# Kernel optimization log

Measured on AMD Instinct MI355X. Metric: run time of the kernel, lower is better.

## Reference

```python
import jax, jax.numpy as jnp
import numpy as np


def setup_inputs() -> dict:
    key = jax.random.key(0)
    ks = jax.random.split(key, 5)
    B, DEC, ENC, H = 4, 256, 256, 512  # feature_dim = hl_size = 512, mlp hidden = 512
    decoder_states = jax.random.normal(ks[0], (B, DEC, H), dtype=jnp.float32)
    encoder_states = jax.random.normal(ks[1], (B, ENC, H), dtype=jnp.float32)
    ext_mask = jnp.zeros((B, DEC, ENC), dtype=bool)  # self.mask set externally; all-False here
    W_mlp = jax.random.normal(ks[2], (2 * H, H), dtype=jnp.float32) * 0.02  # Linear(2H -> H)
    b_mlp = jnp.zeros((H,), dtype=jnp.float32)
    W_out = jax.random.normal(ks[3], (H, 1), dtype=jnp.float32) * 0.02  # Linear(H -> 1)
    b_out = jnp.zeros((1,), dtype=jnp.float32)
    return {"decoder_states": decoder_states, "encoder_states": encoder_states,
            "ext_mask": ext_mask, "W_mlp": W_mlp, "b_mlp": b_mlp,
            "W_out": W_out, "b_out": b_out}


def reference(decoder_states, encoder_states, ext_mask, W_mlp, b_mlp, W_out, b_out):
    # decoder_states: [B, dec, H]; encoder_states: [B, enc, H]
    H = encoder_states.shape[-1]
    # pad mask: positions where encoder feature-0 equals 0.0 -> [B, 1, enc]
    pad_mask = (encoder_states == 0.0)[:, :, :1]
    pad_mask = jnp.swapaxes(pad_mask, 1, 2)  # [B, 1, enc]
    # cat(enc, dec) @ W_mlp  ==  enc @ W_mlp[:H] + dec @ W_mlp[H:]  (avoids 2H concat)
    enc_proj = jnp.einsum('beh,hm->bem', encoder_states, W_mlp[:H])   # [B, enc, Hm]
    dec_proj = jnp.einsum('bdh,hm->bdm', decoder_states, W_mlp[H:])   # [B, dec, Hm]
    hidden = jnp.tanh(dec_proj[:, :, None, :] + enc_proj[:, None, :, :] + b_mlp)  # [B, dec, enc, Hm]
    attn = jnp.einsum('bdem,mo->bde', hidden, W_out) + b_out[0]       # [B, dec, enc]
    attn = jnp.where(ext_mask, -jnp.inf, attn)
    attn = jnp.where(pad_mask, -jnp.inf, attn)
    attn = jax.nn.softmax(attn, axis=-1)
    context = jnp.einsum('bde,beh->bdh', attn, encoder_states)        # [B, dec, H]
    return (context, attn)
```

## Files before the change

### kernel.cpp

```cpp
#include <hip/hip_runtime.h>
#include <math.h>

#define B 4
#define DEC 256
#define ENC 256
#define HDIM 512

#define TANH_SCALE 2.8853900817779268f
#define LOG2E 1.4426950408889634f

__device__ __forceinline__ float fast_exp2(float x) { return __builtin_amdgcn_exp2f(x); }
__device__ __forceinline__ float fast_rcp(float x)  { return __builtin_amdgcn_rcpf(x); }

typedef __attribute__((ext_vector_type(8))) short bf16x8;
typedef __attribute__((ext_vector_type(4))) short bf16x4;
typedef __attribute__((ext_vector_type(4))) float f32x4;

__device__ __forceinline__ unsigned short bf16_rne(float x) {
    unsigned u = __float_as_uint(x);
    return (unsigned short)((u + 0x7FFFu + ((u >> 16) & 1u)) >> 16);
}
__device__ __forceinline__ float bf16_to_f(unsigned short h) {
    return __uint_as_float((unsigned)h << 16);
}

#define W_OFS(m, k) ((((long)(m) >> 4) << 13) + (((long)(k) >> 3) << 7) + (((m) & 15) << 3) + ((k) & 7))

__global__ __launch_bounds__(256) void convert_kernel(
    const float* __restrict__ enc, const float* __restrict__ dec,
    const float* __restrict__ Wmlp,
    unsigned short* __restrict__ Xh_e, unsigned short* __restrict__ Xl_e,
    unsigned short* __restrict__ Xh_d, unsigned short* __restrict__ Xl_d,
    unsigned short* __restrict__ Wh_e, unsigned short* __restrict__ Wl_e,
    unsigned short* __restrict__ Wh_d, unsigned short* __restrict__ Wl_d)
{
    const int tid = threadIdx.x, z = blockIdx.z;
    if (z < 2) {
        const float* X = z ? dec : enc;
        unsigned short* H = z ? Xh_d : Xh_e;
        unsigned short* L = z ? Xl_d : Xl_e;
        const long i8 = ((long)blockIdx.x * 256 + tid) * 8;
        float4 v0 = *(const float4*)(X + i8);
        float4 v1 = *(const float4*)(X + i8 + 4);
        float xs[8] = {v0.x, v0.y, v0.z, v0.w, v1.x, v1.y, v1.z, v1.w};
        bf16x8 hv, lv;
#pragma unroll
        for (int j = 0; j < 8; ++j) {
            unsigned short h = bf16_rne(xs[j]);
            hv[j] = (short)h;
            lv[j] = (short)bf16_rne(xs[j] - bf16_to_f(h));
        }
        *(bf16x8*)(H + i8) = hv;
        *(bf16x8*)(L + i8) = lv;
    } else {
        const float* Wsrc = Wmlp + (z == 3 ? (long)HDIM * HDIM : 0);
        unsigned short* H = (z == 3) ? Wh_d : Wh_e;
        unsigned short* L = (z == 3) ? Wl_d : Wl_e;
        const int t = blockIdx.x * 256 + tid;
        const int m = t & 511;
        const int k0 = (t >> 9) << 2;
        bf16x4 hv, lv;
#pragma unroll
        for (int j = 0; j < 4; ++j) {
            float x = Wsrc[(long)(k0 + j) * 512 + m];
            unsigned short h = bf16_rne(x);
            hv[j] = (short)h;
            lv[j] = (short)bf16_rne(x - bf16_to_f(h));
        }
        const long ofs = W_OFS(m, k0);
        *(bf16x4*)(H + ofs) = hv;
        *(bf16x4*)(L + ofs) = lv;
    }
}

__global__ __launch_bounds__(256) void proj_mfma_kernel(
    const unsigned short* __restrict__ Xh_e, const unsigned short* __restrict__ Xl_e,
    const unsigned short* __restrict__ Xh_d, const unsigned short* __restrict__ Xl_d,
    const unsigned short* __restrict__ Wh_e, const unsigned short* __restrict__ Wl_e,
    const unsigned short* __restrict__ Wh_d, const unsigned short* __restrict__ Wl_d,
    const float* __restrict__ bmlp,
    float* __restrict__ ET, float* __restrict__ Dmat)
{
    const int tid = threadIdx.x;
    const int wave = tid >> 6, lane = tid & 63;
    const int z = blockIdx.z;
    const int r0w = blockIdx.x * 64 + wave * 16;
    const int m0 = blockIdx.y * 32;
    const unsigned short* Xh = z ? Xh_d : Xh_e;
    const unsigned short* Xl = z ? Xl_d : Xl_e;
    const unsigned short* Wh = z ? Wh_d : Wh_e;
    const unsigned short* Wl = z ? Wl_d : Wl_e;

    const int col = lane & 15;
    const int quad = lane >> 4;

    const unsigned short* pah = Xh + (long)(r0w + col) * 512 + quad * 8;
    const unsigned short* pal = Xl + (long)(r0w + col) * 512 + quad * 8;
    const long bofs = ((long)(m0 >> 4) << 13) + (quad << 7) + (col << 3);
    const unsigned short* pb0h = Wh + bofs;
    const unsigned short* pb0l = Wl + bofs;
    const unsigned short* pb1h = Wh + bofs + 8192;
    const unsigned short* pb1l = Wl + bofs + 8192;

    f32x4 a0h = {0.f,0.f,0.f,0.f}, a0x = {0.f,0.f,0.f,0.f};
    f32x4 a1h = {0.f,0.f,0.f,0.f}, a1x = {0.f,0.f,0.f,0.f};

    bf16x8 Ah = *(const bf16x8*)pah,  Al = *(const bf16x8*)pal;
    bf16x8 B0h = *(const bf16x8*)pb0h, B0l = *(const bf16x8*)pb0l;
    bf16x8 B1h = *(const bf16x8*)pb1h, B1l = *(const bf16x8*)pb1l;

#pragma unroll 1
    for (int k0 = 0; k0 < 512; k0 += 32) {
        bf16x8 nAh = Ah, nAl = Al, nB0h = B0h, nB0l = B0l, nB1h = B1h, nB1l = B1l;
        if (k0 + 32 < 512) {
            nAh = *(const bf16x8*)(pah + k0 + 32);
            nAl = *(const bf16x8*)(pal + k0 + 32);
            const long ko = (long)(k0 + 32) << 4;
            nB0h = *(const bf16x8*)(pb0h + ko);
            nB0l = *(const bf16x8*)(pb0l + ko);
            nB1h = *(const bf16x8*)(pb1h + ko);
            nB1l = *(const bf16x8*)(pb1l + ko);
        }
        a0h = __builtin_amdgcn_mfma_f32_16x16x32_bf16(Ah, B0h, a0h, 0, 0, 0);
        a1h = __builtin_amdgcn_mfma_f32_16x16x32_bf16(Ah, B1h, a1h, 0, 0, 0);
        a0x = __builtin_amdgcn_mfma_f32_16x16x32_bf16(Ah, B0l, a0x, 0, 0, 0);
        a1x = __builtin_amdgcn_mfma_f32_16x16x32_bf16(Ah, B1l, a1x, 0, 0, 0);
        a0x = __builtin_amdgcn_mfma_f32_16x16x32_bf16(Al, B0h, a0x, 0, 0, 0);
        a1x = __builtin_amdgcn_mfma_f32_16x16x32_bf16(Al, B1h, a1x, 0, 0, 0);
        Ah = nAh; Al = nAl; B0h = nB0h; B0l = nB0l; B1h = nB1h; B1l = nB1l;
    }

    if (z == 0) {
        const int batch = r0w >> 8;
        const int e0 = (r0w & 255) + quad * 4;
        float* base = ET + (long)batch * HDIM * ENC;
        float4 v;
        v.x = fast_exp2((a0h[0] + a0x[0]) * TANH_SCALE);
        v.y = fast_exp2((a0h[1] + a0x[1]) * TANH_SCALE);
        v.z = fast_exp2((a0h[2] + a0x[2]) * TANH_SCALE);
        v.w = fast_exp2((a0h[3] + a0x[3]) * TANH_SCALE);
        *(float4*)&base[(long)(m0 + col) * ENC + e0] = v;
        v.x = fast_exp2((a1h[0] + a1x[0]) * TANH_SCALE);
        v.y = fast_exp2((a1h[1] + a1x[1]) * TANH_SCALE);
        v.z = fast_exp2((a1h[2] + a1x[2]) * TANH_SCALE);
        v.w = fast_exp2((a1h[3] + a1x[3]) * TANH_SCALE);
        *(float4*)&base[(long)(m0 + 16 + col) * ENC + e0] = v;
    } else {
        const float bq0 = bmlp[m0 + col];
        const float bq1 = bmlp[m0 + 16 + col];
        const int r = r0w + quad * 4;
#pragma unroll
        for (int i = 0; i < 4; ++i) {
            Dmat[(long)(r + i) * HDIM + m0 + col] =
                fast_exp2((a0h[i] + a0x[i] + bq0) * TANH_SCALE);
            Dmat[(long)(r + i) * HDIM + m0 + 16 + col] =
                fast_exp2((a1h[i] + a1x[i] + bq1) * TANH_SCALE);
        }
    }
}

__global__ __launch_bounds__(512) void attn_ctx_kernel(
    const float* __restrict__ Dmat, const float* __restrict__ ET,
    const float* __restrict__ wo,
    const float* __restrict__ enc, const unsigned char* __restrict__ extm,
    float* __restrict__ attn_out, float* __restrict__ ctx)
{
    __shared__ __align__(16) float ds[4][HDIM];
    __shared__ __align__(16) float wos[HDIM];
    __shared__ __align__(16) float p8[8][4][ENC];
    __shared__ __align__(16) float as4T[ENC][4];
    __shared__ float redm[4][4];
    __shared__ float reds[4][4];

    const int tid = threadIdx.x;
    const int b = blockIdx.z, d0 = blockIdx.x * 4;
    const long g0 = (long)b * DEC + d0;

    ((float4*)ds)[tid] = ((const float4*)(Dmat + g0 * HDIM))[tid];
    if (tid < 128) ((float4*)wos)[tid] = ((const float4*)wo)[tid];

    const int mg = tid >> 6;
    const int e4 = (tid & 63) * 4;
    const int mbase = mg * 64;
    const float* ep = ET + (long)b * HDIM * ENC + (long)mbase * ENC + e4;

    float4 E0 = *(const float4*)(ep);
    float4 E1 = *(const float4*)(ep + ENC);
    __syncthreads();

    float acc[4][4] = {};
    for (int i = 0; i < 64; i += 2) {
        float4 Ea = E0, Eb = E1;
        if (i + 2 < 64) {
            E0 = *(const float4*)(ep + (long)(i + 2) * ENC);
            E1 = *(const float4*)(ep + (long)(i + 3) * ENC);
        }
        const int m = mbase + i;
        const float w0 = wos[m], w1 = wos[m + 1];
#pragma unroll
        for (int r = 0; r < 4; ++r) {
            const float dr0 = ds[r][m];
            const float dr1 = ds[r][m + 1];
#pragma unroll
            for (int j = 0; j < 4; ++j) {
                float ea = ((const float*)&Ea)[j];
                float eb = ((const float*)&Eb)[j];
                acc[r][j] = fmaf(w0, fast_rcp(fmaf(ea, dr0, 1.0f)), acc[r][j]);
                acc[r][j] = fmaf(w1, fast_rcp(fmaf(eb, dr1, 1.0f)), acc[r][j]);
            }
        }
    }
#pragma unroll
    for (int r = 0; r < 4; ++r) {
        float4 v = make_float4(acc[r][0], acc[r][1], acc[r][2], acc[r][3]);
        *(float4*)&p8[mg][r][e4] = v;
    }
    __syncthreads();

    const int ty = tid >> 8;
    const int e = tid & 255;
    const int wave = tid >> 6, lane = tid & 63;

    const bool pad = (enc[((long)b * ENC + e) * HDIM] == 0.0f);
    float l[2], p[2];
#pragma unroll
    for (int rl = 0; rl < 2; ++rl) {
        const int r = ty * 2 + rl;
        float a = 0.f;
#pragma unroll
        for (int q = 0; q < 8; ++q) a += p8[q][r][e];
        const bool xm = extm[(g0 + r) * ENC + e] != 0;
        l[rl] = (pad || xm) ? -__builtin_inff() : -2.0f * a;
    }
    float mx[2] = {l[0], l[1]};
#pragma unroll
    for (int off = 32; off >= 1; off >>= 1) {
#pragma unroll
        for (int rl = 0; rl < 2; ++rl)
            mx[rl] = fmaxf(mx[rl], __shfl_xor(mx[rl], off, 64));
    }
    if (lane == 0) {
        redm[ty * 2 + 0][wave & 3] = mx[0];
        redm[ty * 2 + 1][wave & 3] = mx[1];
    }
    __syncthreads();
    float s[2];
#pragma unroll
    for (int rl = 0; rl < 2; ++rl) {
        const int r = ty * 2 + rl;
        const float gm = fmaxf(fmaxf(redm[r][0], redm[r][1]),
                               fmaxf(redm[r][2], redm[r][3]));
        p[rl] = fast_exp2((l[rl] - gm) * LOG2E);
        s[rl] = p[rl];
    }
#pragma unroll
    for (int off = 32; off >= 1; off >>= 1) {
#pragma unroll
        for (int rl = 0; rl < 2; ++rl)
            s[rl] += __shfl_xor(s[rl], off, 64);
    }
    if (lane == 0) {
        reds[ty * 2 + 0][wave & 3] = s[0];
        reds[ty * 2 + 1][wave & 3] = s[1];
    }
    __syncthreads();
#pragma unroll
    for (int rl = 0; rl < 2; ++rl) {
        const int r = ty * 2 + rl;
        const float gs = reds[r][0] + reds[r][1] + reds[r][2] + reds[r][3];
        const float pr = p[rl] * fast_rcp(gs);
        attn_out[(g0 + r) * ENC + e] = pr;
        as4T[e][r] = pr;
    }
    __syncthreads();

    const int h = tid;
    const float* eh = enc + (long)b * ENC * HDIM + h;
    float ac0 = 0.f, ac1 = 0.f, ac2 = 0.f, ac3 = 0.f;
    float ebuf[8], nbuf[8];
#pragma unroll
    for (int j = 0; j < 8; ++j) ebuf[j] = eh[(long)j * HDIM];
    for (int e0 = 0; e0 < ENC; e0 += 8) {
        if (e0 + 8 < ENC) {
#pragma unroll
            for (int j = 0; j < 8; ++j) nbuf[j] = eh[(long)(e0 + 8 + j) * HDIM];
        }
#pragma unroll
        for (int j = 0; j < 8; ++j) {
            float4 prv = *(const float4*)&as4T[e0 + j][0];
            float ev4 = ebuf[j];
            ac0 = fmaf(prv.x, ev4, ac0);
            ac1 = fmaf(prv.y, ev4, ac1);
            ac2 = fmaf(prv.z, ev4, ac2);
            ac3 = fmaf(prv.w, ev4, ac3);
        }
#pragma unroll
        for (int j = 0; j < 8; ++j) ebuf[j] = nbuf[j];
    }
    ctx[(g0 + 0) * HDIM + h] = ac0;
    ctx[(g0 + 1) * HDIM + h] = ac1;
    ctx[(g0 + 2) * HDIM + h] = ac2;
    ctx[(g0 + 3) * HDIM + h] = ac3;
}

extern "C" void kernel_launch(void* const* d_in, const int* in_sizes, int n_in,
                              void* d_out, int out_size, void* d_ws, size_t ws_size,
                              hipStream_t stream) {
    const float* dec = (const float*)d_in[0];
    const float* enc = (const float*)d_in[1];
    const unsigned char* extm = (const unsigned char*)d_in[2];
    const float* Wmlp = (const float*)d_in[3];
    const float* bmlp = (const float*)d_in[4];
    const float* Wout = (const float*)d_in[5];

    float* ctx = (float*)d_out;
    float* attn = ctx + (size_t)B * DEC * HDIM;

    const size_t F = (size_t)B * DEC * HDIM;
    float* ET = (float*)d_ws;
    float* Dmat = ET + F;
    unsigned short* Xh_e = (unsigned short*)(Dmat + F);
    unsigned short* Xl_e = Xh_e + F;
    unsigned short* Xh_d = Xl_e + F;
    unsigned short* Xl_d = Xh_d + F;
    unsigned short* Wh_e = Xl_d + F;
    unsigned short* Wl_e = Wh_e + HDIM * HDIM;
    unsigned short* Wh_d = Wl_e + HDIM * HDIM;
    unsigned short* Wl_d = Wh_d + HDIM * HDIM;

    convert_kernel<<<dim3(256, 1, 4), 256, 0, stream>>>(
        enc, dec, Wmlp, Xh_e, Xl_e, Xh_d, Xl_d, Wh_e, Wl_e, Wh_d, Wl_d);
    proj_mfma_kernel<<<dim3(16, 16, 2), 256, 0, stream>>>(
        Xh_e, Xl_e, Xh_d, Xl_d, Wh_e, Wl_e, Wh_d, Wl_d, bmlp, ET, Dmat);
    attn_ctx_kernel<<<dim3(DEC / 4, 1, B), 512, 0, stream>>>(
        Dmat, ET, Wout, enc, extm, attn, ctx);
}
```

Before: 116.1 us.

## Split context GEMV over encoder quarters with float4 loads and rotate chunk order

The context stage now gives each thread four hidden columns over one quarter of the encoder positions, loading encoder rows as float4. Partial sums go into the reused shared buffer and are then reduced across the four quarters, replacing per-thread scalar strided loads over all 256 positions. The score loop gets deeper prefetch (four rows in flight) and float2 shared loads. Both loops rotate their chunk start by block index to spread concurrent blocks across memory, at the cost of more registers and an extra barrier.

```diff
diff --git a/kernel.cpp b/kernel.cpp
--- a/kernel.cpp
+++ b/kernel.cpp
@@ -167,7 +167,7 @@
 {
     __shared__ __align__(16) float ds[4][HDIM];
     __shared__ __align__(16) float wos[HDIM];
-    __shared__ __align__(16) float p8[8][4][ENC];
+    __shared__ __align__(16) float pbuf[8][4][ENC];
     __shared__ __align__(16) float as4T[ENC][4];
     __shared__ float redm[4][4];
     __shared__ float reds[4][4];
@@ -175,45 +175,48 @@
     const int tid = threadIdx.x;
     const int b = blockIdx.z, d0 = blockIdx.x * 4;
     const long g0 = (long)b * DEC + d0;
+    const int rot = blockIdx.x >> 3;
 
     ((float4*)ds)[tid] = ((const float4*)(Dmat + g0 * HDIM))[tid];
     if (tid < 128) ((float4*)wos)[tid] = ((const float4*)wo)[tid];
 
-    const int mg = tid >> 6;
+    const int mg = ((tid >> 6) + rot) & 7;
     const int e4 = (tid & 63) * 4;
     const int mbase = mg * 64;
     const float* ep = ET + (long)b * HDIM * ENC + (long)mbase * ENC + e4;
 
-    float4 E0 = *(const float4*)(ep);
-    float4 E1 = *(const float4*)(ep + ENC);
+    float4 Eb0 = *(const float4*)(ep);
+    float4 Eb1 = *(const float4*)(ep + ENC);
+    float4 Eb2 = *(const float4*)(ep + 2 * ENC);
+    float4 Eb3 = *(const float4*)(ep + 3 * ENC);
     __syncthreads();
 
     float acc[4][4] = {};
     for (int i = 0; i < 64; i += 2) {
-        float4 Ea = E0, Eb = E1;
-        if (i + 2 < 64) {
-            E0 = *(const float4*)(ep + (long)(i + 2) * ENC);
-            E1 = *(const float4*)(ep + (long)(i + 3) * ENC);
+        float4 Ea = Eb0, Eb = Eb1;
+        Eb0 = Eb2; Eb1 = Eb3;
+        if (i + 4 < 64) {
+            Eb2 = *(const float4*)(ep + (long)(i + 4) * ENC);
+            Eb3 = *(const float4*)(ep + (long)(i + 5) * ENC);
         }
         const int m = mbase + i;
-        const float w0 = wos[m], w1 = wos[m + 1];
+        const float2 w2 = *(const float2*)&wos[m];
 #pragma unroll
         for (int r = 0; r < 4; ++r) {
-            const float dr0 = ds[r][m];
-            const float dr1 = ds[r][m + 1];
+            const float2 d2 = *(const float2*)&ds[r][m];
 #pragma unroll
             for (int j = 0; j < 4; ++j) {
                 float ea = ((const float*)&Ea)[j];
                 float eb = ((const float*)&Eb)[j];
-                acc[r][j] = fmaf(w0, fast_rcp(fmaf(ea, dr0, 1.0f)), acc[r][j]);
-                acc[r][j] = fmaf(w1, fast_rcp(fmaf(eb, dr1, 1.0f)), acc[r][j]);
+                acc[r][j] = fmaf(w2.x, fast_rcp(fmaf(ea, d2.x, 1.0f)), acc[r][j]);
+                acc[r][j] = fmaf(w2.y, fast_rcp(fmaf(eb, d2.y, 1.0f)), acc[r][j]);
             }
         }
     }
 #pragma unroll
     for (int r = 0; r < 4; ++r) {
         float4 v = make_float4(acc[r][0], acc[r][1], acc[r][2], acc[r][3]);
-        *(float4*)&p8[mg][r][e4] = v;
+        *(float4*)&pbuf[mg][r][e4] = v;
     }
     __syncthreads();
 
@@ -228,7 +231,7 @@
         const int r = ty * 2 + rl;
         float a = 0.f;
 #pragma unroll
-        for (int q = 0; q < 8; ++q) a += p8[q][r][e];
+        for (int q = 0; q < 8; ++q) a += pbuf[q][r][e];
         const bool xm = extm[(g0 + r) * ENC + e] != 0;
         l[rl] = (pad || xm) ? -__builtin_inff() : -2.0f * a;
     }
@@ -274,33 +277,50 @@
     }
     __syncthreads();
 
+    float (*p4c)[4][HDIM] = (float (*)[4][HDIM])pbuf;
+
+    const int hq = (tid & 127) * 4;
+    const int eq = ((tid >> 7) + rot) & 3;
+    const int ebase = eq * 64;
+    const float* ew = enc + (long)b * ENC * HDIM + (long)ebase * HDIM + hq;
+
+    float4 Wb0 = *(const float4*)(ew);
+    float4 Wb1 = *(const float4*)(ew + HDIM);
+    float4 Wb2 = *(const float4*)(ew + 2 * HDIM);
+    float4 Wb3 = *(const float4*)(ew + 3 * HDIM);
+
+    float a4[4][4] = {};
+    for (int i = 0; i < 64; i += 2) {
+        float4 Wa = Wb0, Wc = Wb1;
+        Wb0 = Wb2; Wb1 = Wb3;
+        if (i + 4 < 64) {
+            Wb2 = *(const float4*)(ew + (long)(i + 4) * HDIM);
+            Wb3 = *(const float4*)(ew + (long)(i + 5) * HDIM);
+        }
+        float4 pa = *(const float4*)&as4T[ebase + i][0];
+        float4 pb = *(const float4*)&as4T[ebase + i + 1][0];
+#pragma unroll
+        for (int r = 0; r < 4; ++r) {
+            const float par = ((const float*)&pa)[r];
+            const float pbr = ((const float*)&pb)[r];
+#pragma unroll
+            for (int j = 0; j < 4; ++j) {
+                a4[r][j] = fmaf(par, ((const float*)&Wa)[j], a4[r][j]);
+                a4[r][j] = fmaf(pbr, ((const float*)&Wc)[j], a4[r][j]);
+            }
+        }
+    }
+#pragma unroll
+    for (int r = 0; r < 4; ++r)
+        *(float4*)&p4c[eq][r][hq] = make_float4(a4[r][0], a4[r][1], a4[r][2], a4[r][3]);
+    __syncthreads();
+
     const int h = tid;
-    const float* eh = enc + (long)b * ENC * HDIM + h;
-    float ac0 = 0.f, ac1 = 0.f, ac2 = 0.f, ac3 = 0.f;
-    float ebuf[8], nbuf[8];
-#pragma unroll
-    for (int j = 0; j < 8; ++j) ebuf[j] = eh[(long)j * HDIM];
-    for (int e0 = 0; e0 < ENC; e0 += 8) {
-        if (e0 + 8 < ENC) {
-#pragma unroll
-            for (int j = 0; j < 8; ++j) nbuf[j] = eh[(long)(e0 + 8 + j) * HDIM];
-        }
-#pragma unroll
-        for (int j = 0; j < 8; ++j) {
-            float4 prv = *(const float4*)&as4T[e0 + j][0];
-            float ev4 = ebuf[j];
-            ac0 = fmaf(prv.x, ev4, ac0);
-            ac1 = fmaf(prv.y, ev4, ac1);
-            ac2 = fmaf(prv.z, ev4, ac2);
-            ac3 = fmaf(prv.w, ev4, ac3);
-        }
-#pragma unroll
-        for (int j = 0; j < 8; ++j) ebuf[j] = nbuf[j];
-    }
-    ctx[(g0 + 0) * HDIM + h] = ac0;
-    ctx[(g0 + 1) * HDIM + h] = ac1;
-    ctx[(g0 + 2) * HDIM + h] = ac2;
-    ctx[(g0 + 3) * HDIM + h] = ac3;
+#pragma unroll
+    for (int r = 0; r < 4; ++r) {
+        const float o = p4c[0][r][h] + p4c[1][r][h] + p4c[2][r][h] + p4c[3][r][h];
+        ctx[(g0 + r) * HDIM + h] = o;
+    }
 }
 
 extern "C" void kernel_launch(void* const* d_in, const int* in_sizes, int n_in,
```

Result: faster. 110.9 us (-4.5%).
